# Optimization experiments

Hardware: AMD Instinct MI355X
Metric: run time of the kernel (lower is better)

## Reference

```python
import jax, jax.numpy as jnp
import numpy as np

B, S, HID, NH = 4, 1024, 1024, 16
DK = HID // NH
SCALE = DK ** -0.5
NEG = -9e15


def setup_inputs() -> dict:
    key = jax.random.key(0)
    ks = jax.random.split(key, 10)
    std = HID ** -0.5
    return {
        "batch": jax.random.normal(ks[0], (B, S, HID), jnp.float32),
        "attn_bias": jax.random.normal(ks[1], (B, NH, S, S), jnp.float32),
        "Wq": jax.random.normal(ks[2], (HID, HID), jnp.float32) * std,
        "bq": jnp.zeros((HID,), jnp.float32),
        "Wk": jax.random.normal(ks[3], (HID, HID), jnp.float32) * std,
        "bk": jnp.zeros((HID,), jnp.float32),
        "Wv": jax.random.normal(ks[4], (HID, HID), jnp.float32) * std,
        "bv": jnp.zeros((HID,), jnp.float32),
        "Wo": jax.random.normal(ks[5], (HID, HID), jnp.float32) * std,
        "bo": jnp.zeros((HID,), jnp.float32),
    }


def reference(batch, attn_bias, Wq, bq, Wk, bk, Wv, bv, Wo, bo):
    b, s, _ = batch.shape
    # QKV projections -> [b, h, s, d]
    q = (batch @ Wq.T + bq).reshape(b, s, NH, DK).transpose(0, 2, 1, 3)
    k = (batch @ Wk.T + bk).reshape(b, s, NH, DK).transpose(0, 2, 1, 3)
    v = (batch @ Wv.T + bv).reshape(b, s, NH, DK).transpose(0, 2, 1, 3)
    # scaled scores [b, h, s, s]
    x = jnp.einsum("bhqd,bhkd->bhqk", q * SCALE, k)
    # custom zero-mask: exact zeros become -9e15
    x = jnp.where(x == 0, jnp.float32(NEG), x)
    x = x + attn_bias
    p = jax.nn.softmax(x, axis=3)  # dropout_rate=0.0 -> identity
    o = jnp.einsum("bhqk,bhkd->bhqd", p, v)
    o = o.transpose(0, 2, 1, 3).reshape(b, s, NH * DK)
    return o @ Wo.T + bo
```

## Files before the change

### kernel.cpp

```cpp
#include <hip/hip_runtime.h>
#include <hip/hip_bf16.h>
#include <stdint.h>
#include <stddef.h>

#define Bd  4
#define Sd  1024
#define Hd  1024
#define NHd 16
#define DKd 64
#define SCALEF 0.125f
#define NEGV  -9.0e15f
#define L2E   1.4426950408889634f

typedef __attribute__((ext_vector_type(8))) short bfrag;
typedef __attribute__((ext_vector_type(4))) float facc;

typedef __attribute__((address_space(1))) const unsigned int ga_u32;
typedef __attribute__((address_space(3))) unsigned int ls_u32;

__device__ __forceinline__ void gload_lds16(const void* g, void* l) {
  __builtin_amdgcn_global_load_lds((ga_u32*)g, (ls_u32*)l, 16, 0, 0);
}

__device__ __forceinline__ unsigned short f2bf(float f) {
  unsigned int u = __float_as_uint(f);
  u += 0x7fffu + ((u >> 16) & 1u);
  return (unsigned short)(u >> 16);
}

__global__ void castk_all(const float* __restrict__ s0, const float* __restrict__ s1,
                          const float* __restrict__ s2, const float* __restrict__ s3,
                          const float* __restrict__ s4,
                          unsigned short* __restrict__ d0, unsigned short* __restrict__ d1,
                          unsigned short* __restrict__ d2, unsigned short* __restrict__ d3,
                          unsigned short* __restrict__ d4) {
  const int id = blockIdx.x;
  const float* s; unsigned short* d; int i;
  if (id < 4096) { s = s0; d = d0; i = id * 256 + threadIdx.x; }
  else {
    const int w = (id - 4096) >> 10;
    s = (w == 0) ? s1 : (w == 1) ? s2 : (w == 2) ? s3 : s4;
    d = (w == 0) ? d1 : (w == 1) ? d2 : (w == 2) ? d3 : d4;
    i = ((id - 4096) & 1023) * 256 + threadIdx.x;
  }
  float4 v = ((const float4*)s)[i];
  ushort4 ov;
  ov.x = f2bf(v.x); ov.y = f2bf(v.y); ov.z = f2bf(v.z); ov.w = f2bf(v.w);
  ((ushort4*)d)[i] = ov;
}

__global__ __launch_bounds__(256, 3)
void gemm_qkv(const unsigned short* __restrict__ A,
              const unsigned short* __restrict__ W0, const unsigned short* __restrict__ W1,
              const unsigned short* __restrict__ W2,
              const float* __restrict__ b0, const float* __restrict__ b1, const float* __restrict__ b2,
              unsigned short* __restrict__ o0, unsigned short* __restrict__ o1, unsigned short* __restrict__ o2) {
  __shared__ __align__(16) unsigned short smem[128 * 136];
  unsigned short* sA = smem;
  unsigned short* sB = smem + 4096;
  const int z = blockIdx.z;
  const unsigned short* Bm = (z == 0) ? W0 : (z == 1) ? W1 : W2;
  const float* bias = (z == 0) ? b0 : (z == 1) ? b1 : b2;
  unsigned short* out = (z == 0) ? o0 : (z == 1) ? o1 : o2;

  const int m0 = blockIdx.x * 128, n0 = blockIdx.y * 128;
  const int tid = threadIdx.x;
  const int wave = tid >> 6, lane = tid & 63;
  const int quad = lane >> 4, l16 = lane & 15;
  const int wm = wave >> 1, wn = wave & 1;

  facc acc[4][4] = {};

  const int j0 = wave * 128 + lane;
  const int j1 = j0 + 64;
  const int row0 = j0 >> 2, ko0 = (j0 & 3) << 3;
  const int row1 = j1 >> 2, ko1 = (j1 & 3) << 3;
  const size_t aoff0 = (size_t)(m0 + row0) * 1024 + ko0;
  const size_t aoff1 = (size_t)(m0 + row1) * 1024 + ko1;
  const size_t boff0 = (size_t)(n0 + row0) * 1024 + ko0;
  const size_t boff1 = (size_t)(n0 + row1) * 1024 + ko1;
  unsigned short* sA0 = sA + (wave * 2 + 0) * 512;
  unsigned short* sA1 = sA + (wave * 2 + 1) * 512;
  unsigned short* sB0 = sB + (wave * 2 + 0) * 512;
  unsigned short* sB1 = sB + (wave * 2 + 1) * 512;

  for (int k0 = 0; k0 < 1024; k0 += 32) {
    gload_lds16(A + aoff0 + k0, sA0);
    gload_lds16(A + aoff1 + k0, sA1);
    gload_lds16(Bm + boff0 + k0, sB0);
    gload_lds16(Bm + boff1 + k0, sB1);
    __syncthreads();
    bfrag af[4], bf[4];
#pragma unroll
    for (int i = 0; i < 4; ++i) af[i] = *(const bfrag*)(sA + (wm * 64 + i * 16 + l16) * 32 + quad * 8);
#pragma unroll
    for (int j = 0; j < 4; ++j) bf[j] = *(const bfrag*)(sB + (wn * 64 + j * 16 + l16) * 32 + quad * 8);
#pragma unroll
    for (int i = 0; i < 4; ++i)
#pragma unroll
      for (int j = 0; j < 4; ++j)
        acc[i][j] = __builtin_amdgcn_mfma_f32_16x16x32_bf16(af[i], bf[j], acc[i][j], 0, 0, 0);
    __syncthreads();
  }

  if (z < 2) {
#pragma unroll
    for (int i = 0; i < 4; ++i)
#pragma unroll
      for (int j = 0; j < 4; ++j) {
        const int col = n0 + wn * 64 + j * 16 + l16;
        const float bv = bias[col];
        const int h = col >> 6, d = col & 63;
#pragma unroll
        for (int r = 0; r < 4; ++r) {
          const int m = m0 + wm * 64 + i * 16 + quad * 4 + r;
          const int b = m >> 10, s = m & 1023;
          out[(((size_t)(b * NHd + h) * Sd) + s) * DKd + d] = f2bf(acc[i][j][r] + bv);
        }
      }
  } else {
    unsigned short* sT = smem;
#pragma unroll
    for (int i = 0; i < 4; ++i)
#pragma unroll
      for (int j = 0; j < 4; ++j) {
        const int col = n0 + wn * 64 + j * 16 + l16;
        const float bv = bias[col];
        const int nrow = wn * 64 + j * 16 + l16;
        const int mbase = wm * 64 + i * 16 + quad * 4;
        ushort4 pk;
        pk.x = f2bf(acc[i][j][0] + bv);
        pk.y = f2bf(acc[i][j][1] + bv);
        pk.z = f2bf(acc[i][j][2] + bv);
        pk.w = f2bf(acc[i][j][3] + bv);
        *(ushort4*)(sT + nrow * 136 + mbase) = pk;
      }
    __syncthreads();
    const int bI = m0 >> 10, s0i = m0 & 1023;
#pragma unroll
    for (int it = 0; it < 8; ++it) {
      const int c = tid + it * 256;
      const int row = c >> 4, mc = (c & 15) * 8;
      bfrag vv = *(const bfrag*)(sT + row * 136 + mc);
      const int col = n0 + row, hh = col >> 6, dd = col & 63;
      *(bfrag*)(out + (((size_t)(bI * NHd + hh) * DKd) + dd) * Sd + s0i + mc) = vv;
    }
  }
}

__global__ __launch_bounds__(256, 3)
void gemm_out(const unsigned short* __restrict__ A, const unsigned short* __restrict__ Bm,
              const float* __restrict__ bias, float* __restrict__ out) {
  __shared__ __align__(16) unsigned short sA[64 * 64];
  __shared__ __align__(16) unsigned short sB[128 * 64];
  const int m0 = blockIdx.x * 64, n0 = blockIdx.y * 128;
  const int tid = threadIdx.x;
  const int wave = tid >> 6, lane = tid & 63;
  const int quad = lane >> 4, l16 = lane & 15;

  facc acc[8] = {};

  const int cA0 = (wave * 2 + 0) * 64 + lane;
  const int cA1 = (wave * 2 + 1) * 64 + lane;
  const int rA0 = cA0 >> 3, kA0 = ((cA0 & 7) ^ (rA0 & 7)) * 8;
  const int rA1 = cA1 >> 3, kA1 = ((cA1 & 7) ^ (rA1 & 7)) * 8;
  const size_t aoff0 = (size_t)(m0 + rA0) * 1024 + kA0;
  const size_t aoff1 = (size_t)(m0 + rA1) * 1024 + kA1;
  size_t boff[4];
#pragma unroll
  for (int i = 0; i < 4; ++i) {
    const int c = (wave * 4 + i) * 64 + lane;
    const int r = c >> 3, kk = ((c & 7) ^ (r & 7)) * 8;
    boff[i] = (size_t)(n0 + r) * 1024 + kk;
  }

  for (int k0 = 0; k0 < 1024; k0 += 64) {
    gload_lds16(A + aoff0 + k0, sA + (wave * 2 + 0) * 512);
    gload_lds16(A + aoff1 + k0, sA + (wave * 2 + 1) * 512);
#pragma unroll
    for (int i = 0; i < 4; ++i)
      gload_lds16(Bm + boff[i] + k0, sB + (wave * 4 + i) * 512);
    __syncthreads();
#pragma unroll
    for (int c2 = 0; c2 < 2; ++c2) {
      const int ko = ((c2 * 4 + quad) ^ (l16 & 7)) * 8;
      bfrag af = *(const bfrag*)(sA + (wave * 16 + l16) * 64 + ko);
#pragma unroll
      for (int j = 0; j < 8; ++j) {
        bfrag bf = *(const bfrag*)(sB + (j * 16 + l16) * 64 + ko);
        acc[j] = __builtin_amdgcn_mfma_f32_16x16x32_bf16(af, bf, acc[j], 0, 0, 0);
      }
    }
    __syncthreads();
  }

#pragma unroll
  for (int j = 0; j < 8; ++j) {
    const int col = n0 + j * 16 + l16;
    const float bv = bias[col];
#pragma unroll
    for (int r = 0; r < 4; ++r) {
      const int m = m0 + wave * 16 + quad * 4 + r;
      out[(size_t)m * 1024 + col] = acc[j][r] + bv;
    }
  }
}

__global__ __launch_bounds__(128, 4)
void attn_kernel(const unsigned short* __restrict__ q,
                 const unsigned short* __restrict__ k,
                 const unsigned short* __restrict__ vt,
                 const float* __restrict__ bias,
                 unsigned short* __restrict__ o)
{
  __shared__ __align__(16) unsigned short sP[2 * 16 * 136];
  const int bh = blockIdx.y;
  const int q0 = blockIdx.x * 32;
  const int tid = threadIdx.x;
  const int wave = tid >> 6, lane = tid & 63;
  const int quad = lane >> 4, l16 = lane & 15;
  const int b = bh >> 4, h = bh & 15;

  const unsigned short* qh = q + (size_t)bh * Sd * DKd;
  const unsigned short* kh = k + (size_t)bh * Sd * DKd;
  const unsigned short* vh = vt + (size_t)bh * DKd * Sd;
  const float* bias_h = bias + (size_t)bh * Sd * Sd;
  const int rq = q0 + wave * 16;
  unsigned short* sPw = sP + wave * 16 * 136;

  bfrag qf[2];
#pragma unroll
  for (int c = 0; c < 2; ++c)
    qf[c] = *(const bfrag*)(qh + (size_t)(rq + l16) * DKd + c * 32 + quad * 8);

  facc oacc[4] = {};
  float lsum[4] = {0.f, 0.f, 0.f, 0.f};
  const float SL2 = SCALEF * L2E;

  float br[4][8];
  const float* bp0 = bias_h + (size_t)(rq + quad * 4) * Sd + l16;
#pragma unroll
  for (int r = 0; r < 4; ++r)
#pragma unroll
    for (int j = 0; j < 8; ++j)
      br[r][j] = bp0[r * Sd + j * 16];

  for (int t = 0; t < 8; ++t) {
    const int k0 = t * 128;
    facc sacc[8] = {};
#pragma unroll
    for (int c = 0; c < 2; ++c)
#pragma unroll
      for (int j = 0; j < 8; ++j) {
        bfrag kf = *(const bfrag*)(kh + (size_t)(k0 + j * 16 + l16) * DKd + c * 32 + quad * 8);
        sacc[j] = __builtin_amdgcn_mfma_f32_16x16x32_bf16(qf[c], kf, sacc[j], 0, 0, 0);
      }
#pragma unroll
    for (int r = 0; r < 4; ++r)
#pragma unroll
      for (int j = 0; j < 8; ++j) {
        const float x = sacc[j][r];
        float e = exp2f(fmaf(x, SL2, br[r][j] * L2E));
        e = (x == 0.0f) ? 0.0f : e;
        sacc[j][r] = e;
        lsum[r] += e;
      }
    if (t < 7) {
      const float* bp = bp0 + k0 + 128;
#pragma unroll
      for (int r = 0; r < 4; ++r)
#pragma unroll
        for (int j = 0; j < 8; ++j)
          br[r][j] = bp[r * Sd + j * 16];
    }
#pragma unroll
    for (int j = 0; j < 8; ++j)
#pragma unroll
      for (int r = 0; r < 4; ++r)
        sPw[(quad * 4 + r) * 136 + j * 16 + l16] = f2bf(sacc[j][r]);
#pragma unroll
    for (int c = 0; c < 4; ++c) {
      bfrag pf = *(const bfrag*)(sPw + l16 * 136 + c * 32 + quad * 8);
#pragma unroll
      for (int n = 0; n < 4; ++n) {
        bfrag vf = *(const bfrag*)(vh + (size_t)(n * 16 + l16) * Sd + k0 + c * 32 + quad * 8);
        oacc[n] = __builtin_amdgcn_mfma_f32_16x16x32_bf16(pf, vf, oacc[n], 0, 0, 0);
      }
    }
  }

#pragma unroll
  for (int r = 0; r < 4; ++r) {
#pragma unroll
    for (int s = 1; s < 16; s <<= 1) lsum[r] += __shfl_xor(lsum[r], s, 64);
  }
#pragma unroll
  for (int r = 0; r < 4; ++r) {
    const float rinv = 1.0f / lsum[r];
    const size_t rowo = (size_t)(b * Sd + rq + quad * 4 + r) * Hd + h * 64;
#pragma unroll
    for (int n = 0; n < 4; ++n)
      o[rowo + n * 16 + l16] = f2bf(oacc[n][r] * rinv);
  }
}

extern "C" void kernel_launch(void* const* d_in, const int* in_sizes, int n_in,
                              void* d_out, int out_size, void* d_ws, size_t ws_size,
                              hipStream_t stream) {
  const float* batch = (const float*)d_in[0];
  const float* attn_bias = (const float*)d_in[1];
  const float* Wq = (const float*)d_in[2];
  const float* bq = (const float*)d_in[3];
  const float* Wk = (const float*)d_in[4];
  const float* bk = (const float*)d_in[5];
  const float* Wv = (const float*)d_in[6];
  const float* bv = (const float*)d_in[7];
  const float* Wo = (const float*)d_in[8];
  const float* bo = (const float*)d_in[9];
  float* out = (float*)d_out;

  unsigned short* ws = (unsigned short*)d_ws;
  unsigned short* Ab  = ws;
  unsigned short* Wqb = Ab  + 4194304;
  unsigned short* Wkb = Wqb + 1048576;
  unsigned short* Wvb = Wkb + 1048576;
  unsigned short* Wob = Wvb + 1048576;
  unsigned short* qb  = Wob + 1048576;
  unsigned short* kb  = qb  + 4194304;
  unsigned short* vtb = kb  + 4194304;
  unsigned short* ob  = vtb + 4194304;

  castk_all<<<8192, 256, 0, stream>>>(batch, Wq, Wk, Wv, Wo, Ab, Wqb, Wkb, Wvb, Wob);
  gemm_qkv<<<dim3(32, 8, 3), 256, 0, stream>>>(Ab, Wqb, Wkb, Wvb, bq, bk, bv, qb, kb, vtb);
  attn_kernel<<<dim3(32, 64), 128, 0, stream>>>(qb, kb, vtb, attn_bias, ob);
  gemm_out<<<dim3(64, 8), 256, 0, stream>>>(ob, Wob, bo, out);
}
```

Before: 542.9 us.

## Apply softmax in A-fragment layout to enable vectorized bias loads

Raw fp32 scores are now staged through LDS before the exponential instead of after. The exp, zero-mask and bias add then run in the PV A-operand layout, where each lane owns 8 contiguous columns of one row. That allows float4 loads of the attention bias, which dominates memory traffic, in place of scattered strided scalar loads. Row sums collapse to one scalar per lane with fewer shuffles. The cost is fp32 LDS traffic and footprint doubling relative to the bf16 staging, plus an extra broadcast shuffle at the end.

```diff
diff --git a/kernel.cpp b/kernel.cpp
--- a/kernel.cpp
+++ b/kernel.cpp
@@ -213,7 +213,7 @@
                  const float* __restrict__ bias,
                  unsigned short* __restrict__ o)
 {
-  __shared__ __align__(16) unsigned short sP[2 * 16 * 136];
+  __shared__ __align__(16) float sS[2][16][132];
   const int bh = blockIdx.y;
   const int q0 = blockIdx.x * 32;
   const int tid = threadIdx.x;
@@ -226,7 +226,7 @@
   const unsigned short* vh = vt + (size_t)bh * DKd * Sd;
   const float* bias_h = bias + (size_t)bh * Sd * Sd;
   const int rq = q0 + wave * 16;
-  unsigned short* sPw = sP + wave * 16 * 136;
+  float (*sSw)[132] = sS[wave];
 
   bfrag qf[2];
 #pragma unroll
@@ -234,16 +234,16 @@
     qf[c] = *(const bfrag*)(qh + (size_t)(rq + l16) * DKd + c * 32 + quad * 8);
 
   facc oacc[4] = {};
-  float lsum[4] = {0.f, 0.f, 0.f, 0.f};
+  float lsum = 0.f;
   const float SL2 = SCALEF * L2E;
 
-  float br[4][8];
-  const float* bp0 = bias_h + (size_t)(rq + quad * 4) * Sd + l16;
-#pragma unroll
-  for (int r = 0; r < 4; ++r)
-#pragma unroll
-    for (int j = 0; j < 8; ++j)
-      br[r][j] = bp0[r * Sd + j * 16];
+  const float* bp = bias_h + (size_t)(rq + l16) * Sd + quad * 8;
+  float4 br[8];
+#pragma unroll
+  for (int c = 0; c < 4; ++c) {
+    br[2 * c]     = *(const float4*)(bp + c * 32);
+    br[2 * c + 1] = *(const float4*)(bp + c * 32 + 4);
+  }
 
   for (int t = 0; t < 8; ++t) {
     const int k0 = t * 128;
@@ -256,47 +256,53 @@
         sacc[j] = __builtin_amdgcn_mfma_f32_16x16x32_bf16(qf[c], kf, sacc[j], 0, 0, 0);
       }
 #pragma unroll
-    for (int r = 0; r < 4; ++r)
-#pragma unroll
-      for (int j = 0; j < 8; ++j) {
-        const float x = sacc[j][r];
-        float e = exp2f(fmaf(x, SL2, br[r][j] * L2E));
-        e = (x == 0.0f) ? 0.0f : e;
-        sacc[j][r] = e;
-        lsum[r] += e;
-      }
-    if (t < 7) {
-      const float* bp = bp0 + k0 + 128;
+    for (int j = 0; j < 8; ++j)
 #pragma unroll
       for (int r = 0; r < 4; ++r)
-#pragma unroll
-        for (int j = 0; j < 8; ++j)
-          br[r][j] = bp[r * Sd + j * 16];
-    }
-#pragma unroll
-    for (int j = 0; j < 8; ++j)
-#pragma unroll
-      for (int r = 0; r < 4; ++r)
-        sPw[(quad * 4 + r) * 136 + j * 16 + l16] = f2bf(sacc[j][r]);
+        sSw[quad * 4 + r][j * 16 + l16] = sacc[j][r];
 #pragma unroll
     for (int c = 0; c < 4; ++c) {
-      bfrag pf = *(const bfrag*)(sPw + l16 * 136 + c * 32 + quad * 8);
+      const float* sp = &sSw[l16][quad * 8 + c * 32];
+      const float4 s0 = *(const float4*)sp;
+      const float4 s1 = *(const float4*)(sp + 4);
+      const float4 b0 = br[2 * c], b1 = br[2 * c + 1];
+      float e0 = exp2f(fmaf(s0.x, SL2, b0.x * L2E)); e0 = (s0.x == 0.f) ? 0.f : e0;
+      float e1 = exp2f(fmaf(s0.y, SL2, b0.y * L2E)); e1 = (s0.y == 0.f) ? 0.f : e1;
+      float e2 = exp2f(fmaf(s0.z, SL2, b0.z * L2E)); e2 = (s0.z == 0.f) ? 0.f : e2;
+      float e3 = exp2f(fmaf(s0.w, SL2, b0.w * L2E)); e3 = (s0.w == 0.f) ? 0.f : e3;
+      float e4 = exp2f(fmaf(s1.x, SL2, b1.x * L2E)); e4 = (s1.x == 0.f) ? 0.f : e4;
+      float e5 = exp2f(fmaf(s1.y, SL2, b1.y * L2E)); e5 = (s1.y == 0.f) ? 0.f : e5;
+      float e6 = exp2f(fmaf(s1.z, SL2, b1.z * L2E)); e6 = (s1.z == 0.f) ? 0.f : e6;
+      float e7 = exp2f(fmaf(s1.w, SL2, b1.w * L2E)); e7 = (s1.w == 0.f) ? 0.f : e7;
+      lsum += ((e0 + e1) + (e2 + e3)) + ((e4 + e5) + (e6 + e7));
+      bfrag pf;
+      pf[0] = (short)f2bf(e0); pf[1] = (short)f2bf(e1);
+      pf[2] = (short)f2bf(e2); pf[3] = (short)f2bf(e3);
+      pf[4] = (short)f2bf(e4); pf[5] = (short)f2bf(e5);
+      pf[6] = (short)f2bf(e6); pf[7] = (short)f2bf(e7);
 #pragma unroll
       for (int n = 0; n < 4; ++n) {
         bfrag vf = *(const bfrag*)(vh + (size_t)(n * 16 + l16) * Sd + k0 + c * 32 + quad * 8);
         oacc[n] = __builtin_amdgcn_mfma_f32_16x16x32_bf16(pf, vf, oacc[n], 0, 0, 0);
       }
     }
-  }
+    if (t < 7) {
+      const float* bpn = bp + k0 + 128;
+#pragma unroll
+      for (int c = 0; c < 4; ++c) {
+        br[2 * c]     = *(const float4*)(bpn + c * 32);
+        br[2 * c + 1] = *(const float4*)(bpn + c * 32 + 4);
+      }
+    }
+  }
+
+  lsum += __shfl_xor(lsum, 16, 64);
+  lsum += __shfl_xor(lsum, 32, 64);
 
 #pragma unroll
   for (int r = 0; r < 4; ++r) {
-#pragma unroll
-    for (int s = 1; s < 16; s <<= 1) lsum[r] += __shfl_xor(lsum[r], s, 64);
-  }
-#pragma unroll
-  for (int r = 0; r < 4; ++r) {
-    const float rinv = 1.0f / lsum[r];
+    const float rs = __shfl(lsum, quad * 4 + r, 64);
+    const float rinv = 1.0f / rs;
     const size_t rowo = (size_t)(b * Sd + rq + quad * 4 + r) * Hd + h * 64;
 #pragma unroll
     for (int n = 0; n < 4; ++n)
```

Result: no change. 534.9 us (-1.5%).
